# Kernel tuning notes

Measured on AMD Instinct MI355X. Metric: run time of the kernel, lower is better.

## Reference

```python
import jax, jax.numpy as jnp
import numpy as np
from jax import lax

B = 64
N_WIRES = 4
NUM_CENTERS = 64


def setup_inputs() -> dict:
    key = jax.random.key(0)
    ks = jax.random.split(key, 17)
    f32 = jnp.float32

    def w(k, shape, fan_in):
        return jax.random.normal(k, shape, dtype=f32) * (1.0 / np.sqrt(fan_in))

    return {
        "x": jax.random.normal(ks[0], (B, 3, 250, 250), dtype=f32),
        # conv backbone
        "conv1_w": w(ks[1], (6, 3, 5, 5), 3 * 25),
        "conv1_b": jnp.zeros((6,), f32),
        "conv2_w": w(ks[2], (15, 6, 3, 3), 6 * 9),
        "conv2_b": jnp.zeros((15,), f32),
        # MLP head of feature extractor
        "fc1_w": w(ks[3], (120, 55815), 55815),
        "fc1_b": jnp.zeros((120,), f32),
        "fc2_w": w(ks[4], (84, 120), 120),
        "fc2_b": jnp.zeros((84,), f32),
        # quantum kernel centers (num_centers, input_dim=84)
        "centers": jax.random.normal(ks[5], (NUM_CENTERS, 84), dtype=f32),
        # classifier: depth=2 hidden layers of width num_centers, then head->2
        "cls_w1": w(ks[6], (NUM_CENTERS, NUM_CENTERS), NUM_CENTERS),
        "cls_b1": jnp.zeros((NUM_CENTERS,), f32),
        "cls_w2": w(ks[7], (NUM_CENTERS, NUM_CENTERS), NUM_CENTERS),
        "cls_b2": jnp.zeros((NUM_CENTERS,), f32),
        "cls_w3": w(ks[8], (2, NUM_CENTERS), NUM_CENTERS),
        "cls_b3": jnp.zeros((2,), f32),
    }


def _maxpool2_s1(h):
    # MaxPool2d(kernel_size=2, stride=1), VALID padding
    return lax.reduce_window(h, -jnp.inf, lax.max, (1, 1, 2, 2), (1, 1, 1, 1), "VALID")


def reference(x, conv1_w, conv1_b, conv2_w, conv2_b, fc1_w, fc1_b, fc2_w, fc2_b,
              centers, cls_w1, cls_b1, cls_w2, cls_b2, cls_w3, cls_b3):
    dn = ("NCHW", "OIHW", "NCHW")
    # Conv(3->6, k5, s2, p1) + ReLU + MaxPool(2, s1)   (dropout = identity in eval)
    h = lax.conv_general_dilated(x, conv1_w, (2, 2), [(1, 1), (1, 1)], dimension_numbers=dn)
    h = jax.nn.relu(h + conv1_b[None, :, None, None])
    h = _maxpool2_s1(h)                                   # [B,6,123,123]
    # Conv(6->15, k3, s2, p1) + ReLU + MaxPool(2, s1)
    h = lax.conv_general_dilated(h, conv2_w, (2, 2), [(1, 1), (1, 1)], dimension_numbers=dn)
    h = jax.nn.relu(h + conv2_b[None, :, None, None])
    h = _maxpool2_s1(h)                                   # [B,15,61,61]
    h = h.reshape(h.shape[0], -1)                         # [B,55815]
    h = jax.nn.relu(h @ fc1_w.T + fc1_b)                  # [B,120]
    feat = jax.nn.relu(h @ fc2_w.T + fc2_b)               # [B,84]

    # Quantum fidelity kernel over n_wires=4 qubits:
    # encode RY(x_i) then RY(-c_i) per wire on |0>, read |0...0| amplitude ->
    # k[b,c] = |prod_i cos((x_i - c_i)/2)| over the first 4 feature dims.
    diff = feat[:, None, :N_WIRES] - centers[None, :, :N_WIRES]  # [B,C,4]
    k = jnp.abs(jnp.prod(jnp.cos(0.5 * diff), axis=-1))          # [B,C]

    h = jax.nn.relu(k @ cls_w1.T + cls_b1)
    h = jax.nn.relu(h @ cls_w2.T + cls_b2)
    logits = h @ cls_w3.T + cls_b3                        # [B,2]
    return jax.nn.softmax(logits, axis=-1)
```

## Files before the change

kernel.cpp:

```cpp
#include <hip/hip_runtime.h>
#include <hip/hip_bf16.h>

typedef float float4a __attribute__((ext_vector_type(4), aligned(4)));
typedef float float2a __attribute__((ext_vector_type(2), aligned(4)));
typedef short bfrag   __attribute__((ext_vector_type(8)));
typedef float f32x4   __attribute__((ext_vector_type(4)));

#define P1W_PAD 128
#define APAD 56064
#define KFC 55815
#define CHUNK 256
#define NCHUNK 219
#define NFC1 120

#define oP1B   ((size_t)0)
#define oAB    ((size_t)24182784)
#define oPARTB ((size_t)38535168)
#define oP2B   ((size_t)45262848)

__global__ __launch_bounds__(256) void conv1_pool(const float* __restrict__ x,
        const float* __restrict__ w, const float* __restrict__ bias,
        float* __restrict__ p1) {
    __shared__ float ex[8 * 6 * 128];
    const int tid = threadIdx.x;
    const int G = blockIdx.x;
    const int b = blockIdx.y;
    const int t = tid >> 5;
    const int s = tid & 31;
    const int r = 7 * G + t;
    const bool act = (r < 124) && (s < 31);

    if (act) {
        float acc[6][4];
        #pragma unroll
        for (int c = 0; c < 6; ++c) {
            const float bz = bias[c];
            #pragma unroll
            for (int j = 0; j < 4; ++j) acc[c][j] = bz;
        }
        for (int ic = 0; ic < 3; ++ic) {
            const float* xpl = x + (size_t)(b * 3 + ic) * 62500;
            #pragma unroll
            for (int ky = 0; ky < 5; ++ky) {
                const int iy = 2 * r - 1 + ky;
                if (iy < 0) continue;
                const float* rp = xpl + iy * 250 + 8 * s;
                float a[11];
                a[0] = (s > 0) ? rp[-1] : 0.f;
                *(float4a*)&a[1] = *(const float4a*)rp;
                *(float4a*)&a[5] = *(const float4a*)(rp + 4);
                *(float2a*)&a[9] = *(const float2a*)(rp + 8);
                const float* wb = w + ic * 25 + ky * 5;
                #pragma unroll
                for (int c = 0; c < 6; ++c) {
                    #pragma unroll
                    for (int kx = 0; kx < 5; ++kx) {
                        const float wv = wb[c * 75 + kx];
                        #pragma unroll
                        for (int j = 0; j < 4; ++j)
                            acc[c][j] = fmaf(a[2 * j + kx], wv, acc[c][j]);
                    }
                }
            }
        }
        #pragma unroll
        for (int c = 0; c < 6; ++c)
            *(float4*)&ex[(t * 6 + c) * 128 + 4 * s] = *(float4*)&acc[c][0];
    }
    __syncthreads();
    const int np = min(7, 123 - 7 * G);
    for (int idx = tid; idx < np * 768; idx += 256) {
        const int p   = idx / 768;
        const int rem = idx - p * 768;
        const int c   = rem >> 7;
        const int pc  = rem & 127;
        float v = 0.f;
        if (pc < 123) {
            const float* r0 = &ex[((p    ) * 6 + c) * 128 + pc];
            const float* r1 = &ex[((p + 1) * 6 + c) * 128 + pc];
            v = fmaxf(fmaxf(fmaxf(r0[0], r0[1]), fmaxf(r1[0], r1[1])), 0.f);
        }
        p1[((size_t)(b * 6 + c) * 123 + (7 * G + p)) * P1W_PAD + pc] = v;
    }
}

__global__ __launch_bounds__(256) void conv2_pool(const float* __restrict__ p1,
        const float* __restrict__ w, const float* __restrict__ bias,
        float* __restrict__ A) {
    __shared__ float ex[16 * 15 * 64];
    const int tid = threadIdx.x;
    const int G = blockIdx.x;
    const int b = blockIdx.y;
    const int t = tid >> 4;
    const int s = tid & 15;
    const int r = 15 * G + t;
    const bool act = (r < 62);

    if (act) {
        float acc[15][4];
        #pragma unroll
        for (int c = 0; c < 15; ++c) {
            const float bz = bias[c];
            #pragma unroll
            for (int j = 0; j < 4; ++j) acc[c][j] = bz;
        }
        for (int ic = 0; ic < 6; ++ic) {
            const float* pl = p1 + (size_t)(b * 6 + ic) * 123 * P1W_PAD;
            #pragma unroll
            for (int ky = 0; ky < 3; ++ky) {
                const int iy = 2 * r - 1 + ky;
                if (iy < 0 || iy > 122) continue;
                const float* rp = pl + iy * P1W_PAD + 8 * s;
                float a[9];
                a[0] = (s > 0) ? rp[-1] : 0.f;
                *(float4a*)&a[1] = *(const float4a*)rp;
                *(float4a*)&a[5] = *(const float4a*)(rp + 4);
                const float* wb = w + ic * 9 + ky * 3;
                #pragma unroll
                for (int c = 0; c < 15; ++c) {
                    #pragma unroll
                    for (int kx = 0; kx < 3; ++kx) {
                        const float wv = wb[c * 54 + kx];
                        #pragma unroll
                        for (int j = 0; j < 4; ++j)
                            acc[c][j] = fmaf(a[2 * j + kx], wv, acc[c][j]);
                    }
                }
            }
        }
        #pragma unroll
        for (int c = 0; c < 15; ++c)
            *(float4*)&ex[(t * 15 + c) * 64 + 4 * s] = *(float4*)&acc[c][0];
    }
    __syncthreads();
    const int np = min(15, 61 - 15 * G);
    for (int idx = tid; idx < np * 915; idx += 256) {
        const int p   = idx / 915;
        const int rem = idx % 915;
        const int c   = rem / 61;
        const int pc  = rem % 61;
        const float* r0 = &ex[((p    ) * 15 + c) * 64 + pc];
        const float* r1 = &ex[((p + 1) * 15 + c) * 64 + pc];
        const float v = fmaxf(fmaxf(r0[0], r0[1]), fmaxf(r1[0], r1[1]));
        A[(size_t)b * APAD + c * 3721 + (15 * G + p) * 61 + pc] = fmaxf(v, 0.f);
    }
    if (G == 0)
        for (int i2 = tid; i2 < 249; i2 += 256)
            A[(size_t)b * APAD + KFC + i2] = 0.f;
}

__global__ __launch_bounds__(256) void fc1_s1(const float* __restrict__ A,
        const float* __restrict__ W, float* __restrict__ part) {
    const int cBlk = blockIdx.x;
    const int nth  = blockIdx.y;
    const int k0 = cBlk * CHUNK;
    const int tid = threadIdx.x;
    const int lane  = tid & 63;
    const int mtile = tid >> 6;
    const int ocol  = lane & 15;
    const int kq    = lane >> 4;
    const int arow  = mtile * 16 + ocol;

    const float* ab = A + (size_t)arow * APAD + k0 + kq * 8;
    const float* wb[4];
    #pragma unroll
    for (int ntl = 0; ntl < 4; ++ntl) {
        const int o = (nth * 4 + ntl) * 16 + ocol;
        wb[ntl] = W + (size_t)min(o, NFC1 - 1) * KFC + k0 + kq * 8;
    }

    f32x4 acc[4];
    #pragma unroll
    for (int n = 0; n < 4; ++n) acc[n] = (f32x4){0.f, 0.f, 0.f, 0.f};

    const bool full = (cBlk != NCHUNK - 1);
    #pragma unroll 2
    for (int ks = 0; ks < 8; ++ks) {
        float af[8];
        *(float4a*)&af[0] = *(const float4a*)(ab + ks * 32);
        *(float4a*)&af[4] = *(const float4a*)(ab + ks * 32 + 4);
        bfrag ah, al;
        #pragma unroll
        for (int e = 0; e < 8; ++e) {
            const unsigned u = __float_as_uint(af[e]);
            ah[e] = (short)(u >> 16);
            const float rres = af[e] - __uint_as_float(u & 0xffff0000u);
            al[e] = (short)(__float_as_uint(rres) >> 16);
        }
        #pragma unroll
        for (int ntl = 0; ntl < 4; ++ntl) {
            float wf[8];
            if (full) {
                *(float4a*)&wf[0] = *(const float4a*)(wb[ntl] + ks * 32);
                *(float4a*)&wf[4] = *(const float4a*)(wb[ntl] + ks * 32 + 4);
            } else {
                const int kg = k0 + ks * 32 + kq * 8;
                #pragma unroll
                for (int e = 0; e < 8; ++e)
                    wf[e] = (kg + e < KFC) ? wb[ntl][ks * 32 + e] : 0.f;
            }
            bfrag wh, wl;
            #pragma unroll
            for (int e = 0; e < 8; ++e) {
                const unsigned u = __float_as_uint(wf[e]);
                wh[e] = (short)(u >> 16);
                const float rres = wf[e] - __uint_as_float(u & 0xffff0000u);
                wl[e] = (short)(__float_as_uint(rres) >> 16);
            }
            acc[ntl] = __builtin_amdgcn_mfma_f32_16x16x32_bf16(ah, wh, acc[ntl], 0, 0, 0);
            acc[ntl] = __builtin_amdgcn_mfma_f32_16x16x32_bf16(al, wh, acc[ntl], 0, 0, 0);
            acc[ntl] = __builtin_amdgcn_mfma_f32_16x16x32_bf16(ah, wl, acc[ntl], 0, 0, 0);
        }
    }
    #pragma unroll
    for (int ntl = 0; ntl < 4; ++ntl) {
        const int o = (nth * 4 + ntl) * 16 + ocol;
        if (o < NFC1) {
            #pragma unroll
            for (int rr = 0; rr < 4; ++rr) {
                const int brow = mtile * 16 + kq * 4 + rr;
                part[((size_t)cBlk * 64 + brow) * NFC1 + o] = acc[ntl][rr];
            }
        }
    }
}

__global__ __launch_bounds__(256) void fc1_s2a(const float* __restrict__ part,
        float* __restrict__ part2) {
    const int idx = blockIdx.x * 256 + threadIdx.x;
    const int seg = idx / 7680;
    const int r   = idx % 7680;
    const int c0 = seg * 27 + min(seg, 3);
    const int n  = 27 + (seg < 3 ? 1 : 0);
    float s = 0.f;
    for (int c = c0; c < c0 + n; ++c) s += part[(size_t)c * 7680 + r];
    part2[idx] = s;
}

__global__ __launch_bounds__(64) void tail_k(const float* __restrict__ part2,
        const float* __restrict__ fc1b,
        const float* __restrict__ fc2w, const float* __restrict__ fc2b,
        const float* __restrict__ centers,
        const float* __restrict__ w1, const float* __restrict__ b1,
        const float* __restrict__ w2, const float* __restrict__ b2,
        const float* __restrict__ w3, const float* __restrict__ b3,
        float* __restrict__ out) {
    const int b = blockIdx.x;
    const int lane = threadIdx.x;
    __shared__ float h[120];
    __shared__ float feat[4];
    __shared__ float bufA[64];
    __shared__ float bufB[64];

    for (int o = lane; o < NFC1; o += 64) {
        float sv = fc1b[o];
        #pragma unroll
        for (int g = 0; g < 8; ++g) sv += part2[g * 7680 + b * NFC1 + o];
        h[o] = fmaxf(sv, 0.f);
    }
    __syncthreads();

    const int j = lane >> 4, p = lane & 15;
    float sv = 0.f;
    for (int o = p; o < NFC1; o += 16) sv = fmaf(fc2w[j * NFC1 + o], h[o], sv);
    #pragma unroll
    for (int off = 8; off; off >>= 1) sv += __shfl_xor(sv, off, 16);
    if (p == 0) feat[j] = fmaxf(sv + fc2b[j], 0.f);
    __syncthreads();

    float prod = 1.f;
    #pragma unroll
    for (int i = 0; i < 4; ++i) prod *= cosf(0.5f * (feat[i] - centers[lane * 84 + i]));
    bufA[lane] = fabsf(prod);
    __syncthreads();

    float s1 = b1[lane];
    for (int jj = 0; jj < 64; ++jj) s1 = fmaf(w1[lane * 64 + jj], bufA[jj], s1);
    bufB[lane] = fmaxf(s1, 0.f);
    __syncthreads();

    float s2 = b2[lane];
    for (int jj = 0; jj < 64; ++jj) s2 = fmaf(w2[lane * 64 + jj], bufB[jj], s2);
    bufA[lane] = fmaxf(s2, 0.f);
    __syncthreads();

    if (lane < 2) {
        float s3 = b3[lane];
        for (int jj = 0; jj < 64; ++jj) s3 = fmaf(w3[lane * 64 + jj], bufA[jj], s3);
        const float other = __shfl_xor(s3, 1, 2);
        const float m = fmaxf(s3, other);
        const float e = expf(s3 - m), eo = expf(other - m);
        out[b * 2 + lane] = e / (e + eo);
    }
}

extern "C" void kernel_launch(void* const* d_in, const int* in_sizes, int n_in,
                              void* d_out, int out_size, void* d_ws, size_t ws_size,
                              hipStream_t stream) {
    const float* x       = (const float*)d_in[0];
    const float* conv1_w = (const float*)d_in[1];
    const float* conv1_b = (const float*)d_in[2];
    const float* conv2_w = (const float*)d_in[3];
    const float* conv2_b = (const float*)d_in[4];
    const float* fc1_w   = (const float*)d_in[5];
    const float* fc1_b   = (const float*)d_in[6];
    const float* fc2_w   = (const float*)d_in[7];
    const float* fc2_b   = (const float*)d_in[8];
    const float* centers = (const float*)d_in[9];
    const float* cls_w1  = (const float*)d_in[10];
    const float* cls_b1  = (const float*)d_in[11];
    const float* cls_w2  = (const float*)d_in[12];
    const float* cls_b2  = (const float*)d_in[13];
    const float* cls_w3  = (const float*)d_in[14];
    const float* cls_b3  = (const float*)d_in[15];
    char* ws = (char*)d_ws;
    float* outp = (float*)d_out;

    float* p1    = (float*)(ws + oP1B);
    float* Abuf  = (float*)(ws + oAB);
    float* partb = (float*)(ws + oPARTB);
    float* part2 = (float*)(ws + oP2B);

    hipLaunchKernelGGL(conv1_pool, dim3(18, 64), dim3(256), 0, stream, x, conv1_w, conv1_b, p1);
    hipLaunchKernelGGL(conv2_pool, dim3(5, 64), dim3(256), 0, stream, p1, conv2_w, conv2_b, Abuf);
    hipLaunchKernelGGL(fc1_s1, dim3(NCHUNK, 2), dim3(256), 0, stream, Abuf, fc1_w, partb);
    hipLaunchKernelGGL(fc1_s2a, dim3(240), dim3(256), 0, stream, partb, part2);
    hipLaunchKernelGGL(tail_k, dim3(64), dim3(64), 0, stream,
                       part2, fc1_b, fc2_w, fc2_b, centers,
                       cls_w1, cls_b1, cls_w2, cls_b2, cls_w3, cls_b3, outp);
}
```

Baseline: 86.00 us.

## Pre-split fc1 operands into bf16 hi/lo fragments in separate kernels

Adds two prepass kernels that convert the fc1 weight and the activation matrix into bf16 hi/lo fragment arrays, laid out in the order the MFMA consumer reads them. The GEMM kernel then loads ready-made fragments instead of converting fp32 data on the fly. The aim is to take the split arithmetic out of the inner loop and make the fragment loads contiguous. In exchange, the weight (about 27 MB) is read, written as split data and read again on every call, and two extra launches are added.

```diff
diff --git a/kernel.cpp b/kernel.cpp
--- a/kernel.cpp
+++ b/kernel.cpp
@@ -15,8 +15,10 @@
 
 #define oP1B   ((size_t)0)
 #define oAB    ((size_t)24182784)
-#define oPARTB ((size_t)38535168)
-#define oP2B   ((size_t)45262848)
+#define oASP   ((size_t)38535168)
+#define oWSP   ((size_t)52887552)
+#define oPARTB ((size_t)81592320)
+#define oP2B   ((size_t)88320000)
 
 __global__ __launch_bounds__(256) void conv1_pool(const float* __restrict__ x,
         const float* __restrict__ w, const float* __restrict__ bias,
@@ -149,11 +151,69 @@
             A[(size_t)b * APAD + KFC + i2] = 0.f;
 }
 
-__global__ __launch_bounds__(256) void fc1_s1(const float* __restrict__ A,
-        const float* __restrict__ W, float* __restrict__ part) {
+__global__ __launch_bounds__(256) void wsplit_k(const float* __restrict__ W, bfrag* __restrict__ Wsp) {
+    const int idx = blockIdx.x * 256 + threadIdx.x;
+    const int kq = idx & 3;
+    const int o  = (idx >> 2) & 127;
+    const int ks = (idx >> 9) & 7;
+    const int cBlk = idx >> 12;
+    const int k0 = cBlk * CHUNK + ks * 32 + kq * 8;
+
+    float wf[8];
+    if (o < NFC1 && k0 + 7 < KFC) {
+        const float* wp = W + (size_t)o * KFC + k0;
+        *(float4a*)&wf[0] = *(const float4a*)wp;
+        *(float4a*)&wf[4] = *(const float4a*)(wp + 4);
+    } else {
+        #pragma unroll
+        for (int e = 0; e < 8; ++e)
+            wf[e] = (o < NFC1 && k0 + e < KFC) ? W[(size_t)o * KFC + k0 + e] : 0.f;
+    }
+    bfrag wh, wl;
+    #pragma unroll
+    for (int e = 0; e < 8; ++e) {
+        const unsigned u = __float_as_uint(wf[e]);
+        wh[e] = (short)(u >> 16);
+        const float rres = wf[e] - __uint_as_float(u & 0xffff0000u);
+        wl[e] = (short)(__float_as_uint(rres) >> 16);
+    }
+    const size_t fh = ((((size_t)cBlk * 8 + ks) * 2 + 0) * 128 + o) * 4 + kq;
+    const size_t fl = ((((size_t)cBlk * 8 + ks) * 2 + 1) * 128 + o) * 4 + kq;
+    Wsp[fh] = wh;
+    Wsp[fl] = wl;
+}
+
+__global__ __launch_bounds__(256) void asplit_k(const float* __restrict__ A, bfrag* __restrict__ Asp) {
+    const int idx = blockIdx.x * 256 + threadIdx.x;
+    const int kq = idx & 3;
+    const int row = (idx >> 2) & 63;
+    const int ks = (idx >> 8) & 7;
+    const int cBlk = idx >> 11;
+    const int k0 = cBlk * CHUNK + ks * 32 + kq * 8;
+
+    const float* ap = A + (size_t)row * APAD + k0;
+    float af[8];
+    *(float4*)&af[0] = *(const float4*)ap;
+    *(float4*)&af[4] = *(const float4*)(ap + 4);
+
+    bfrag ah, al;
+    #pragma unroll
+    for (int e = 0; e < 8; ++e) {
+        const unsigned u = __float_as_uint(af[e]);
+        ah[e] = (short)(u >> 16);
+        const float rres = af[e] - __uint_as_float(u & 0xffff0000u);
+        al[e] = (short)(__float_as_uint(rres) >> 16);
+    }
+    const size_t fh = ((((size_t)cBlk * 8 + ks) * 2 + 0) * 64 + row) * 4 + kq;
+    const size_t fl = ((((size_t)cBlk * 8 + ks) * 2 + 1) * 64 + row) * 4 + kq;
+    Asp[fh] = ah;
+    Asp[fl] = al;
+}
+
+__global__ __launch_bounds__(256) void fc1_s1(const bfrag* __restrict__ Asp,
+        const bfrag* __restrict__ Wsp, float* __restrict__ part) {
     const int cBlk = blockIdx.x;
     const int nth  = blockIdx.y;
-    const int k0 = cBlk * CHUNK;
     const int tid = threadIdx.x;
     const int lane  = tid & 63;
     const int mtile = tid >> 6;
@@ -161,52 +221,22 @@
     const int kq    = lane >> 4;
     const int arow  = mtile * 16 + ocol;
 
-    const float* ab = A + (size_t)arow * APAD + k0 + kq * 8;
-    const float* wb[4];
-    #pragma unroll
-    for (int ntl = 0; ntl < 4; ++ntl) {
-        const int o = (nth * 4 + ntl) * 16 + ocol;
-        wb[ntl] = W + (size_t)min(o, NFC1 - 1) * KFC + k0 + kq * 8;
-    }
+    const bfrag* Ab = Asp + (size_t)cBlk * (8 * 2 * 64 * 4);
+    const bfrag* Wb = Wsp + (size_t)cBlk * (8 * 2 * 128 * 4);
 
     f32x4 acc[4];
     #pragma unroll
     for (int n = 0; n < 4; ++n) acc[n] = (f32x4){0.f, 0.f, 0.f, 0.f};
 
-    const bool full = (cBlk != NCHUNK - 1);
-    #pragma unroll 2
+    #pragma unroll
     for (int ks = 0; ks < 8; ++ks) {
-        float af[8];
-        *(float4a*)&af[0] = *(const float4a*)(ab + ks * 32);
-        *(float4a*)&af[4] = *(const float4a*)(ab + ks * 32 + 4);
-        bfrag ah, al;
-        #pragma unroll
-        for (int e = 0; e < 8; ++e) {
-            const unsigned u = __float_as_uint(af[e]);
-            ah[e] = (short)(u >> 16);
-            const float rres = af[e] - __uint_as_float(u & 0xffff0000u);
-            al[e] = (short)(__float_as_uint(rres) >> 16);
-        }
+        const bfrag ah = Ab[((ks * 2 + 0) * 64 + arow) * 4 + kq];
+        const bfrag al = Ab[((ks * 2 + 1) * 64 + arow) * 4 + kq];
         #pragma unroll
         for (int ntl = 0; ntl < 4; ++ntl) {
-            float wf[8];
-            if (full) {
-                *(float4a*)&wf[0] = *(const float4a*)(wb[ntl] + ks * 32);
-                *(float4a*)&wf[4] = *(const float4a*)(wb[ntl] + ks * 32 + 4);
-            } else {
-                const int kg = k0 + ks * 32 + kq * 8;
-                #pragma unroll
-                for (int e = 0; e < 8; ++e)
-                    wf[e] = (kg + e < KFC) ? wb[ntl][ks * 32 + e] : 0.f;
-            }
-            bfrag wh, wl;
-            #pragma unroll
-            for (int e = 0; e < 8; ++e) {
-                const unsigned u = __float_as_uint(wf[e]);
-                wh[e] = (short)(u >> 16);
-                const float rres = wf[e] - __uint_as_float(u & 0xffff0000u);
-                wl[e] = (short)(__float_as_uint(rres) >> 16);
-            }
+            const int o = nth * 64 + ntl * 16 + ocol;
+            const bfrag wh = Wb[((ks * 2 + 0) * 128 + o) * 4 + kq];
+            const bfrag wl = Wb[((ks * 2 + 1) * 128 + o) * 4 + kq];
             acc[ntl] = __builtin_amdgcn_mfma_f32_16x16x32_bf16(ah, wh, acc[ntl], 0, 0, 0);
             acc[ntl] = __builtin_amdgcn_mfma_f32_16x16x32_bf16(al, wh, acc[ntl], 0, 0, 0);
             acc[ntl] = __builtin_amdgcn_mfma_f32_16x16x32_bf16(ah, wl, acc[ntl], 0, 0, 0);
@@ -214,7 +244,7 @@
     }
     #pragma unroll
     for (int ntl = 0; ntl < 4; ++ntl) {
-        const int o = (nth * 4 + ntl) * 16 + ocol;
+        const int o = nth * 64 + ntl * 16 + ocol;
         if (o < NFC1) {
             #pragma unroll
             for (int rr = 0; rr < 4; ++rr) {
@@ -318,12 +348,16 @@
 
     float* p1    = (float*)(ws + oP1B);
     float* Abuf  = (float*)(ws + oAB);
+    bfrag* Aspl  = (bfrag*)(ws + oASP);
+    bfrag* Wspl  = (bfrag*)(ws + oWSP);
     float* partb = (float*)(ws + oPARTB);
     float* part2 = (float*)(ws + oP2B);
 
+    hipLaunchKernelGGL(wsplit_k, dim3(3504), dim3(256), 0, stream, fc1_w, Wspl);
     hipLaunchKernelGGL(conv1_pool, dim3(18, 64), dim3(256), 0, stream, x, conv1_w, conv1_b, p1);
     hipLaunchKernelGGL(conv2_pool, dim3(5, 64), dim3(256), 0, stream, p1, conv2_w, conv2_b, Abuf);
-    hipLaunchKernelGGL(fc1_s1, dim3(NCHUNK, 2), dim3(256), 0, stream, Abuf, fc1_w, partb);
+    hipLaunchKernelGGL(asplit_k, dim3(1752), dim3(256), 0, stream, Abuf, Aspl);
+    hipLaunchKernelGGL(fc1_s1, dim3(NCHUNK, 2), dim3(256), 0, stream, Aspl, Wspl, partb);
     hipLaunchKernelGGL(fc1_s2a, dim3(240), dim3(256), 0, stream, partb, part2);
     hipLaunchKernelGGL(tail_k, dim3(64), dim3(64), 0, stream,
                        part2, fc1_b, fc2_w, fc2_b, centers,
```

Result: slower. 101.0 us (+17.4%).

## Widen conv1 per-thread tiles with in-register pooling and split conv2 channels across grid

Applied to the files above, without the earlier changes.

In conv1, each thread now computes 9 overlapping output columns (16 input columns) instead of 4, and the horizontal max of the pool is taken in registers before staging to LDS. The block shrinks to 128 threads, and the LDS pass now only does the vertical max. This cuts redundant input loads and LDS traffic, but raises register pressure and halves the threads per block. Separately, conv2 splits its 15 output channels into three grid slices of 5 to reduce per-thread accumulators and LDS, adding parallelism at the cost of re-reading the input three times.

```diff
diff --git a/kernel.cpp b/kernel.cpp
--- a/kernel.cpp
+++ b/kernel.cpp
@@ -18,38 +18,48 @@
 #define oPARTB ((size_t)38535168)
 #define oP2B   ((size_t)45262848)
 
-__global__ __launch_bounds__(256) void conv1_pool(const float* __restrict__ x,
+__global__ __launch_bounds__(128) void conv1_pool(const float* __restrict__ x,
         const float* __restrict__ w, const float* __restrict__ bias,
         float* __restrict__ p1) {
     __shared__ float ex[8 * 6 * 128];
     const int tid = threadIdx.x;
     const int G = blockIdx.x;
     const int b = blockIdx.y;
-    const int t = tid >> 5;
-    const int s = tid & 31;
+    const int t = tid >> 4;
+    const int s = tid & 15;
     const int r = 7 * G + t;
-    const bool act = (r < 124) && (s < 31);
-
-    if (act) {
-        float acc[6][4];
+
+    if (r < 124) {
+        float acc[6][9];
         #pragma unroll
         for (int c = 0; c < 6; ++c) {
             const float bz = bias[c];
             #pragma unroll
-            for (int j = 0; j < 4; ++j) acc[c][j] = bz;
-        }
+            for (int j = 0; j < 9; ++j) acc[c][j] = bz;
+        }
+        const int c0 = 16 * s;
         for (int ic = 0; ic < 3; ++ic) {
             const float* xpl = x + (size_t)(b * 3 + ic) * 62500;
             #pragma unroll
             for (int ky = 0; ky < 5; ++ky) {
                 const int iy = 2 * r - 1 + ky;
                 if (iy < 0) continue;
-                const float* rp = xpl + iy * 250 + 8 * s;
-                float a[11];
+                const float* rp = xpl + iy * 250 + c0;
+                float a[21];
                 a[0] = (s > 0) ? rp[-1] : 0.f;
-                *(float4a*)&a[1] = *(const float4a*)rp;
-                *(float4a*)&a[5] = *(const float4a*)(rp + 4);
-                *(float2a*)&a[9] = *(const float2a*)(rp + 8);
+                if (s < 15) {
+                    *(float4a*)&a[1]  = *(const float4a*)rp;
+                    *(float4a*)&a[5]  = *(const float4a*)(rp + 4);
+                    *(float4a*)&a[9]  = *(const float4a*)(rp + 8);
+                    *(float4a*)&a[13] = *(const float4a*)(rp + 12);
+                    *(float4a*)&a[17] = *(const float4a*)(rp + 16);
+                } else {
+                    *(float4a*)&a[1]  = *(const float4a*)rp;
+                    *(float4a*)&a[5]  = *(const float4a*)(rp + 4);
+                    *(float2a*)&a[9]  = *(const float2a*)(rp + 8);
+                    #pragma unroll
+                    for (int k = 11; k < 21; ++k) a[k] = 0.f;
+                }
                 const float* wb = w + ic * 25 + ky * 5;
                 #pragma unroll
                 for (int c = 0; c < 6; ++c) {
@@ -57,50 +67,57 @@
                     for (int kx = 0; kx < 5; ++kx) {
                         const float wv = wb[c * 75 + kx];
                         #pragma unroll
-                        for (int j = 0; j < 4; ++j)
+                        for (int j = 0; j < 9; ++j)
                             acc[c][j] = fmaf(a[2 * j + kx], wv, acc[c][j]);
                     }
                 }
             }
         }
         #pragma unroll
-        for (int c = 0; c < 6; ++c)
-            *(float4*)&ex[(t * 6 + c) * 128 + 4 * s] = *(float4*)&acc[c][0];
-    }
-    __syncthreads();
-    const int np = min(7, 123 - 7 * G);
-    for (int idx = tid; idx < np * 768; idx += 256) {
+        for (int c = 0; c < 6; ++c) {
+            float cm[8];
+            #pragma unroll
+            for (int pc = 0; pc < 8; ++pc)
+                cm[pc] = fmaxf(acc[c][pc], acc[c][pc + 1]);
+            *(float4*)&ex[(t * 6 + c) * 128 + 8 * s]     = *(float4*)&cm[0];
+            *(float4*)&ex[(t * 6 + c) * 128 + 8 * s + 4] = *(float4*)&cm[4];
+        }
+    }
+    __syncthreads();
+    for (int idx = tid; idx < 7 * 768; idx += 128) {
         const int p   = idx / 768;
         const int rem = idx - p * 768;
         const int c   = rem >> 7;
         const int pc  = rem & 127;
-        float v = 0.f;
-        if (pc < 123) {
-            const float* r0 = &ex[((p    ) * 6 + c) * 128 + pc];
-            const float* r1 = &ex[((p + 1) * 6 + c) * 128 + pc];
-            v = fmaxf(fmaxf(fmaxf(r0[0], r0[1]), fmaxf(r1[0], r1[1])), 0.f);
-        }
-        p1[((size_t)(b * 6 + c) * 123 + (7 * G + p)) * P1W_PAD + pc] = v;
+        const int pr  = 7 * G + p;
+        if (pr < 123) {
+            float v = 0.f;
+            if (pc < 123)
+                v = fmaxf(fmaxf(ex[(p * 6 + c) * 128 + pc],
+                                ex[((p + 1) * 6 + c) * 128 + pc]), 0.f);
+            p1[((size_t)(b * 6 + c) * 123 + pr) * P1W_PAD + pc] = v;
+        }
     }
 }
 
 __global__ __launch_bounds__(256) void conv2_pool(const float* __restrict__ p1,
         const float* __restrict__ w, const float* __restrict__ bias,
         float* __restrict__ A) {
-    __shared__ float ex[16 * 15 * 64];
+    __shared__ float ex[16 * 5 * 64];
     const int tid = threadIdx.x;
     const int G = blockIdx.x;
     const int b = blockIdx.y;
+    const int cb = blockIdx.z * 5;
     const int t = tid >> 4;
     const int s = tid & 15;
     const int r = 15 * G + t;
     const bool act = (r < 62);
 
     if (act) {
-        float acc[15][4];
-        #pragma unroll
-        for (int c = 0; c < 15; ++c) {
-            const float bz = bias[c];
+        float acc[5][4];
+        #pragma unroll
+        for (int c = 0; c < 5; ++c) {
+            const float bz = bias[cb + c];
             #pragma unroll
             for (int j = 0; j < 4; ++j) acc[c][j] = bz;
         }
@@ -117,10 +134,10 @@
                 *(float4a*)&a[5] = *(const float4a*)(rp + 4);
                 const float* wb = w + ic * 9 + ky * 3;
                 #pragma unroll
-                for (int c = 0; c < 15; ++c) {
+                for (int c = 0; c < 5; ++c) {
                     #pragma unroll
                     for (int kx = 0; kx < 3; ++kx) {
-                        const float wv = wb[c * 54 + kx];
+                        const float wv = wb[(cb + c) * 54 + kx];
                         #pragma unroll
                         for (int j = 0; j < 4; ++j)
                             acc[c][j] = fmaf(a[2 * j + kx], wv, acc[c][j]);
@@ -129,22 +146,22 @@
             }
         }
         #pragma unroll
-        for (int c = 0; c < 15; ++c)
-            *(float4*)&ex[(t * 15 + c) * 64 + 4 * s] = *(float4*)&acc[c][0];
+        for (int c = 0; c < 5; ++c)
+            *(float4*)&ex[(t * 5 + c) * 64 + 4 * s] = *(float4*)&acc[c][0];
     }
     __syncthreads();
     const int np = min(15, 61 - 15 * G);
-    for (int idx = tid; idx < np * 915; idx += 256) {
-        const int p   = idx / 915;
-        const int rem = idx % 915;
+    for (int idx = tid; idx < np * 305; idx += 256) {
+        const int p   = idx / 305;
+        const int rem = idx % 305;
         const int c   = rem / 61;
         const int pc  = rem % 61;
-        const float* r0 = &ex[((p    ) * 15 + c) * 64 + pc];
-        const float* r1 = &ex[((p + 1) * 15 + c) * 64 + pc];
+        const float* r0 = &ex[((p    ) * 5 + c) * 64 + pc];
+        const float* r1 = &ex[((p + 1) * 5 + c) * 64 + pc];
         const float v = fmaxf(fmaxf(r0[0], r0[1]), fmaxf(r1[0], r1[1]));
-        A[(size_t)b * APAD + c * 3721 + (15 * G + p) * 61 + pc] = fmaxf(v, 0.f);
-    }
-    if (G == 0)
+        A[(size_t)b * APAD + (cb + c) * 3721 + (15 * G + p) * 61 + pc] = fmaxf(v, 0.f);
+    }
+    if (G == 0 && cb == 0)
         for (int i2 = tid; i2 < 249; i2 += 256)
             A[(size_t)b * APAD + KFC + i2] = 0.f;
 }
@@ -321,8 +338,8 @@
     float* partb = (float*)(ws + oPARTB);
     float* part2 = (float*)(ws + oP2B);
 
-    hipLaunchKernelGGL(conv1_pool, dim3(18, 64), dim3(256), 0, stream, x, conv1_w, conv1_b, p1);
-    hipLaunchKernelGGL(conv2_pool, dim3(5, 64), dim3(256), 0, stream, p1, conv2_w, conv2_b, Abuf);
+    hipLaunchKernelGGL(conv1_pool, dim3(18, 64), dim3(128), 0, stream, x, conv1_w, conv1_b, p1);
+    hipLaunchKernelGGL(conv2_pool, dim3(5, 64, 3), dim3(256), 0, stream, p1, conv2_w, conv2_b, Abuf);
     hipLaunchKernelGGL(fc1_s1, dim3(NCHUNK, 2), dim3(256), 0, stream, Abuf, fc1_w, partb);
     hipLaunchKernelGGL(fc1_s2a, dim3(240), dim3(256), 0, stream, partb, part2);
     hipLaunchKernelGGL(tail_k, dim3(64), dim3(64), 0, stream,
```

Result: slower. 96.01 us (+11.6%).

## Split conv2 output channels across grid z and fold fc1 reduction into tail

Applied to the files above, without the earlier changes.

conv2_pool now processes 5 of the 15 output channels per block, using a third grid dimension. This triples the block count, cuts per-thread accumulator registers and shrinks shared memory, which should improve occupancy on a grid that was only 320 blocks. The separate fc1_s2a partial-sum kernel is removed: tail_k now runs 256 threads and reduces the 219 fc1 chunks directly, with two threads per output. That saves one launch and an intermediate buffer, but the tail reduction uses only 64 blocks and strided reads, so it may be slower per block.

```diff
diff --git a/kernel.cpp b/kernel.cpp
--- a/kernel.cpp
+++ b/kernel.cpp
@@ -16,7 +16,6 @@
 #define oP1B   ((size_t)0)
 #define oAB    ((size_t)24182784)
 #define oPARTB ((size_t)38535168)
-#define oP2B   ((size_t)45262848)
 
 __global__ __launch_bounds__(256) void conv1_pool(const float* __restrict__ x,
         const float* __restrict__ w, const float* __restrict__ bias,
@@ -87,20 +86,21 @@
 __global__ __launch_bounds__(256) void conv2_pool(const float* __restrict__ p1,
         const float* __restrict__ w, const float* __restrict__ bias,
         float* __restrict__ A) {
-    __shared__ float ex[16 * 15 * 64];
+    __shared__ float ex[16 * 5 * 64];
     const int tid = threadIdx.x;
     const int G = blockIdx.x;
     const int b = blockIdx.y;
+    const int cb = blockIdx.z * 5;
     const int t = tid >> 4;
     const int s = tid & 15;
     const int r = 15 * G + t;
     const bool act = (r < 62);
 
     if (act) {
-        float acc[15][4];
-        #pragma unroll
-        for (int c = 0; c < 15; ++c) {
-            const float bz = bias[c];
+        float acc[5][4];
+        #pragma unroll
+        for (int c = 0; c < 5; ++c) {
+            const float bz = bias[cb + c];
             #pragma unroll
             for (int j = 0; j < 4; ++j) acc[c][j] = bz;
         }
@@ -117,10 +117,10 @@
                 *(float4a*)&a[5] = *(const float4a*)(rp + 4);
                 const float* wb = w + ic * 9 + ky * 3;
                 #pragma unroll
-                for (int c = 0; c < 15; ++c) {
+                for (int c = 0; c < 5; ++c) {
                     #pragma unroll
                     for (int kx = 0; kx < 3; ++kx) {
-                        const float wv = wb[c * 54 + kx];
+                        const float wv = wb[(cb + c) * 54 + kx];
                         #pragma unroll
                         for (int j = 0; j < 4; ++j)
                             acc[c][j] = fmaf(a[2 * j + kx], wv, acc[c][j]);
@@ -129,22 +129,22 @@
             }
         }
         #pragma unroll
-        for (int c = 0; c < 15; ++c)
-            *(float4*)&ex[(t * 15 + c) * 64 + 4 * s] = *(float4*)&acc[c][0];
+        for (int c = 0; c < 5; ++c)
+            *(float4*)&ex[(t * 5 + c) * 64 + 4 * s] = *(float4*)&acc[c][0];
     }
     __syncthreads();
     const int np = min(15, 61 - 15 * G);
-    for (int idx = tid; idx < np * 915; idx += 256) {
-        const int p   = idx / 915;
-        const int rem = idx % 915;
+    for (int idx = tid; idx < np * 305; idx += 256) {
+        const int p   = idx / 305;
+        const int rem = idx % 305;
         const int c   = rem / 61;
         const int pc  = rem % 61;
-        const float* r0 = &ex[((p    ) * 15 + c) * 64 + pc];
-        const float* r1 = &ex[((p + 1) * 15 + c) * 64 + pc];
+        const float* r0 = &ex[((p    ) * 5 + c) * 64 + pc];
+        const float* r1 = &ex[((p + 1) * 5 + c) * 64 + pc];
         const float v = fmaxf(fmaxf(r0[0], r0[1]), fmaxf(r1[0], r1[1]));
-        A[(size_t)b * APAD + c * 3721 + (15 * G + p) * 61 + pc] = fmaxf(v, 0.f);
-    }
-    if (G == 0)
+        A[(size_t)b * APAD + (cb + c) * 3721 + (15 * G + p) * 61 + pc] = fmaxf(v, 0.f);
+    }
+    if (G == 0 && cb == 0)
         for (int i2 = tid; i2 < 249; i2 += 256)
             A[(size_t)b * APAD + KFC + i2] = 0.f;
 }
@@ -225,19 +225,7 @@
     }
 }
 
-__global__ __launch_bounds__(256) void fc1_s2a(const float* __restrict__ part,
-        float* __restrict__ part2) {
-    const int idx = blockIdx.x * 256 + threadIdx.x;
-    const int seg = idx / 7680;
-    const int r   = idx % 7680;
-    const int c0 = seg * 27 + min(seg, 3);
-    const int n  = 27 + (seg < 3 ? 1 : 0);
-    float s = 0.f;
-    for (int c = c0; c < c0 + n; ++c) s += part[(size_t)c * 7680 + r];
-    part2[idx] = s;
-}
-
-__global__ __launch_bounds__(64) void tail_k(const float* __restrict__ part2,
+__global__ __launch_bounds__(256) void tail_k(const float* __restrict__ part,
         const float* __restrict__ fc1b,
         const float* __restrict__ fc2w, const float* __restrict__ fc2b,
         const float* __restrict__ centers,
@@ -246,51 +234,63 @@
         const float* __restrict__ w3, const float* __restrict__ b3,
         float* __restrict__ out) {
     const int b = blockIdx.x;
-    const int lane = threadIdx.x;
+    const int tid = threadIdx.x;
+    __shared__ float partial[240];
     __shared__ float h[120];
     __shared__ float feat[4];
     __shared__ float bufA[64];
     __shared__ float bufB[64];
 
-    for (int o = lane; o < NFC1; o += 64) {
-        float sv = fc1b[o];
-        #pragma unroll
-        for (int g = 0; g < 8; ++g) sv += part2[g * 7680 + b * NFC1 + o];
-        h[o] = fmaxf(sv, 0.f);
-    }
-    __syncthreads();
-
-    const int j = lane >> 4, p = lane & 15;
-    float sv = 0.f;
-    for (int o = p; o < NFC1; o += 16) sv = fmaf(fc2w[j * NFC1 + o], h[o], sv);
-    #pragma unroll
-    for (int off = 8; off; off >>= 1) sv += __shfl_xor(sv, off, 16);
-    if (p == 0) feat[j] = fmaxf(sv + fc2b[j], 0.f);
-    __syncthreads();
-
-    float prod = 1.f;
-    #pragma unroll
-    for (int i = 0; i < 4; ++i) prod *= cosf(0.5f * (feat[i] - centers[lane * 84 + i]));
-    bufA[lane] = fabsf(prod);
-    __syncthreads();
-
-    float s1 = b1[lane];
-    for (int jj = 0; jj < 64; ++jj) s1 = fmaf(w1[lane * 64 + jj], bufA[jj], s1);
-    bufB[lane] = fmaxf(s1, 0.f);
-    __syncthreads();
-
-    float s2 = b2[lane];
-    for (int jj = 0; jj < 64; ++jj) s2 = fmaf(w2[lane * 64 + jj], bufB[jj], s2);
-    bufA[lane] = fmaxf(s2, 0.f);
-    __syncthreads();
-
-    if (lane < 2) {
-        float s3 = b3[lane];
-        for (int jj = 0; jj < 64; ++jj) s3 = fmaf(w3[lane * 64 + jj], bufA[jj], s3);
+    if (tid < 240) {
+        const int o  = tid % 120;
+        const int hf = tid / 120;
+        const int c0 = hf ? 110 : 0;
+        const int c1 = hf ? 219 : 110;
+        float sacc = 0.f;
+        for (int c = c0; c < c1; ++c)
+            sacc += part[((size_t)c * 64 + b) * NFC1 + o];
+        partial[tid] = sacc;
+    }
+    __syncthreads();
+    if (tid < 120) h[tid] = fmaxf(partial[tid] + partial[120 + tid] + fc1b[tid], 0.f);
+    __syncthreads();
+
+    if (tid < 64) {
+        const int j = tid >> 4, p = tid & 15;
+        float sv = 0.f;
+        for (int o = p; o < NFC1; o += 16) sv = fmaf(fc2w[j * NFC1 + o], h[o], sv);
+        #pragma unroll
+        for (int off = 8; off; off >>= 1) sv += __shfl_xor(sv, off, 16);
+        if (p == 0) feat[j] = fmaxf(sv + fc2b[j], 0.f);
+    }
+    __syncthreads();
+
+    if (tid < 64) {
+        float prod = 1.f;
+        #pragma unroll
+        for (int i = 0; i < 4; ++i) prod *= cosf(0.5f * (feat[i] - centers[tid * 84 + i]));
+        bufA[tid] = fabsf(prod);
+    }
+    __syncthreads();
+    if (tid < 64) {
+        float s1 = b1[tid];
+        for (int jj = 0; jj < 64; ++jj) s1 = fmaf(w1[tid * 64 + jj], bufA[jj], s1);
+        bufB[tid] = fmaxf(s1, 0.f);
+    }
+    __syncthreads();
+    if (tid < 64) {
+        float s2 = b2[tid];
+        for (int jj = 0; jj < 64; ++jj) s2 = fmaf(w2[tid * 64 + jj], bufB[jj], s2);
+        bufA[tid] = fmaxf(s2, 0.f);
+    }
+    __syncthreads();
+    if (tid < 2) {
+        float s3 = b3[tid];
+        for (int jj = 0; jj < 64; ++jj) s3 = fmaf(w3[tid * 64 + jj], bufA[jj], s3);
         const float other = __shfl_xor(s3, 1, 2);
         const float m = fmaxf(s3, other);
         const float e = expf(s3 - m), eo = expf(other - m);
-        out[b * 2 + lane] = e / (e + eo);
+        out[b * 2 + tid] = e / (e + eo);
     }
 }
 
@@ -319,13 +319,11 @@
     float* p1    = (float*)(ws + oP1B);
     float* Abuf  = (float*)(ws + oAB);
     float* partb = (float*)(ws + oPARTB);
-    float* part2 = (float*)(ws + oP2B);
 
     hipLaunchKernelGGL(conv1_pool, dim3(18, 64), dim3(256), 0, stream, x, conv1_w, conv1_b, p1);
-    hipLaunchKernelGGL(conv2_pool, dim3(5, 64), dim3(256), 0, stream, p1, conv2_w, conv2_b, Abuf);
+    hipLaunchKernelGGL(conv2_pool, dim3(5, 64, 3), dim3(256), 0, stream, p1, conv2_w, conv2_b, Abuf);
     hipLaunchKernelGGL(fc1_s1, dim3(NCHUNK, 2), dim3(256), 0, stream, Abuf, fc1_w, partb);
-    hipLaunchKernelGGL(fc1_s2a, dim3(240), dim3(256), 0, stream, partb, part2);
-    hipLaunchKernelGGL(tail_k, dim3(64), dim3(64), 0, stream,
-                       part2, fc1_b, fc2_w, fc2_b, centers,
+    hipLaunchKernelGGL(tail_k, dim3(64), dim3(256), 0, stream,
+                       partb, fc1_b, fc2_w, fc2_b, centers,
                        cls_w1, cls_b1, cls_w2, cls_b2, cls_w3, cls_b3, outp);
 }
```

Result: slower. 100.9 us (+17.3%).
